# Performance work log

Hardware: AMD Instinct MI355X
Metric: run time of the kernel (lower is better)

## Reference

```python
import jax, jax.numpy as jnp
import numpy as np

EPS = 1e-5
NUM_GROUPS = 32
NUM_HEADS = 8

def group_norm(x, w, b):
    # x: (B, C, H, W), 32 groups, affine per-channel
    B, C, H, W = x.shape
    xg = x.reshape(B, NUM_GROUPS, C // NUM_GROUPS, H, W)
    mu = xg.mean(axis=(2, 3, 4), keepdims=True)
    var = xg.var(axis=(2, 3, 4), keepdims=True)
    xn = ((xg - mu) * jax.lax.rsqrt(var + EPS)).reshape(B, C, H, W)
    return xn * w[None, :, None, None] + b[None, :, None, None]

def conv1x1(x, w, b):
    # 1x1 conv == per-pixel linear; w: (out, in), x: (B, C, H, W)
    return jnp.einsum('oc,bchw->bohw', w, x) + b[None, :, None, None]

def setup_inputs() -> dict:
    key = jax.random.key(0)
    ks = jax.random.split(key, 4)
    B, C, H, W = 2, 512, 64, 64
    s = 1.0 / np.sqrt(C)
    return {
        'x': jax.random.normal(ks[0], (B, C, H, W), jnp.float32),
        'gn_w': jnp.ones((C,), jnp.float32),
        'gn_b': jnp.zeros((C,), jnp.float32),
        'wq': jax.random.normal(ks[1], (C, C), jnp.float32) * s,
        'bq': jnp.zeros((C,), jnp.float32),
        'wkv': jax.random.normal(ks[2], (2 * C, C), jnp.float32) * s,
        'bkv': jnp.zeros((2 * C,), jnp.float32),
        'wo': jax.random.normal(ks[3], (C, C), jnp.float32) * s,
        'bo': jnp.zeros((C,), jnp.float32),
    }

def reference(x, gn_w, gn_b, wq, bq, wkv, bkv, wo, bo):
    B, C, H, W = x.shape
    hd = C // NUM_HEADS  # head_dim
    residual = x
    x_norm = group_norm(x, gn_w, gn_b)
    q = conv1x1(x_norm, wq, bq).reshape(B, NUM_HEADS, hd, H * W)
    kv = conv1x1(x_norm, wkv, bkv)
    k, v = jnp.split(kv, 2, axis=1)
    k = k.reshape(B, NUM_HEADS, hd, H * W)
    v = v.reshape(B, NUM_HEADS, hd, H * W)
    scale = hd ** (-0.5)
    attn = jnp.einsum('bhdi,bhdj->bhij', q, k) * scale
    attn = jax.nn.softmax(attn, axis=-1)
    out = jnp.einsum('bhij,bhdj->bhdi', attn, v).reshape(B, C, H, W)
    out = conv1x1(out, wo, bo)
    return out + residual
```

## Files before the change

kernel.cpp:

```cpp
#include <hip/hip_runtime.h>
#include <cmath>

typedef __bf16 bf16x8 __attribute__((ext_vector_type(8)));
typedef __bf16 bf16x4 __attribute__((ext_vector_type(4)));
typedef float  f32x4  __attribute__((ext_vector_type(4)));
typedef unsigned uint2_ev __attribute__((ext_vector_type(2)));

static __device__ __forceinline__ f32x4 mfma16(bf16x8 a, bf16x8 b, f32x4 c) {
    return __builtin_amdgcn_mfma_f32_16x16x32_bf16(a, b, c, 0, 0, 0);
}

static __device__ __forceinline__ float fast_exp2(float x) {
#if __has_builtin(__builtin_amdgcn_exp2f)
    return __builtin_amdgcn_exp2f(x);
#else
    return exp2f(x);
#endif
}

static __device__ __forceinline__ void quad_swap(unsigned &a, unsigned &b) {
#if __has_builtin(__builtin_amdgcn_permlane32_swap) && __has_builtin(__builtin_amdgcn_permlane16_swap)
    uint2_ev r32 = __builtin_amdgcn_permlane32_swap(a, b, false, false);
    uint2_ev r16 = __builtin_amdgcn_permlane16_swap(r32[0], r32[1], false, false);
    a = r16[0]; b = r16[1];
#else
    asm volatile("v_permlane32_swap_b32 %0, %1\n\t"
                 "v_permlane16_swap_b32 %0, %1"
                 : "+v"(a), "+v"(b));
#endif
}

static __device__ __forceinline__ void gload_lds16(const void* g, void* l) {
    __builtin_amdgcn_global_load_lds((const __attribute__((address_space(1))) void*)g,
                                     (__attribute__((address_space(3))) void*)l, 16, 0, 0);
}

#define OFF_STATS 0
#define OFF_W     4096
#define OFF_XNT   (OFF_W + 2u*1024*1024)
#define OFF_QKT   (OFF_XNT + 8u*1024*1024)
#define OFF_V     (OFF_QKT + 16u*1024*1024)
#define OFF_OP    (OFF_V + 8u*1024*1024)
#define CHUNK_O   4194304u
#define CHUNK_L   65536u

__global__ __launch_bounds__(256) void cvt_w(const float* __restrict__ wq,
                                             const float* __restrict__ wkv,
                                             const float* __restrict__ wo,
                                             __bf16* __restrict__ dst) {
    int i = blockIdx.x * 256 + threadIdx.x;
    if (i < 262144)      dst[i] = (__bf16)wq[i];
    else if (i < 786432) dst[i] = (__bf16)wkv[i - 262144];
    else                 dst[i] = (__bf16)wo[i - 786432];
}

__global__ __launch_bounds__(256) void gn_stats(const float* __restrict__ x,
                                                float* __restrict__ stats) {
    int blk = blockIdx.x;
    int bg = blk >> 2, chunk = blk & 3;
    const float* base = x + (size_t)bg * 65536 + (size_t)chunk * 16384;
    float s = 0.f, ss = 0.f;
    for (int i = threadIdx.x; i < 4096; i += 256) {
        float4 v = ((const float4*)base)[i];
        s  += v.x + v.y + v.z + v.w;
        ss += v.x*v.x + v.y*v.y + v.z*v.z + v.w*v.w;
    }
    #pragma unroll
    for (int off = 1; off < 64; off <<= 1) {
        s  += __shfl_xor(s,  off);
        ss += __shfl_xor(ss, off);
    }
    __shared__ float red[8];
    int wave = threadIdx.x >> 6;
    if ((threadIdx.x & 63) == 0) { red[wave*2] = s; red[wave*2+1] = ss; }
    __syncthreads();
    if (threadIdx.x == 0) {
        float S  = red[0] + red[2] + red[4] + red[6];
        float SS = red[1] + red[3] + red[5] + red[7];
        atomicAdd(&stats[bg*2],     S);
        atomicAdd(&stats[bg*2 + 1], SS);
    }
}

__global__ __launch_bounds__(256) void gn_apply(const float* __restrict__ x,
                                                const float* __restrict__ stats,
                                                const float* __restrict__ w,
                                                const float* __restrict__ bgn,
                                                __bf16* __restrict__ xnT) {
    int p0 = blockIdx.x * 64, c0 = blockIdx.y * 64, b = blockIdx.z;
    int tid = threadIdx.x, lane = tid & 63, wave = tid >> 6;
    __shared__ float t[64][69];
    #pragma unroll
    for (int i = 0; i < 16; ++i) {
        int cc = i * 4 + wave;
        int c  = c0 + cc;
        int g  = (b << 5) + (c >> 4);
        float mu  = stats[g*2] * (1.f/65536.f);
        float var = stats[g*2+1] * (1.f/65536.f) - mu*mu;
        float rstd = rsqrtf(var + 1e-5f);
        float val = x[((size_t)(b*512 + c) << 12) + p0 + lane];
        t[cc][lane] = (val - mu) * rstd * w[c] + bgn[c];
    }
    __syncthreads();
    #pragma unroll
    for (int i = 0; i < 16; ++i) {
        int pp = i * 4 + wave;
        xnT[((size_t)(b*4096 + p0 + pp) << 9) + c0 + lane] = (__bf16)t[lane][pp];
    }
}

__global__ __launch_bounds__(256) void gemm128_kernel(
    const __bf16* __restrict__ A, const __bf16* __restrict__ B,
    const float* __restrict__ bias, const float* __restrict__ bias2, int nsplit,
    float scale0, void* __restrict__ out,
    int N, int K, long long strideA, long long strideO) {
    const int bz = blockIdx.z;
    A += strideA * bz;
    const int m0 = blockIdx.x * 128, n0 = blockIdx.y * 128;
    const int tid = threadIdx.x, lane = tid & 63, wave = tid >> 6;
    const int quad = lane >> 4, l16 = lane & 15;
    const int wm = (wave >> 1) * 64, wn = (wave & 1) * 64;

    __shared__ __attribute__((aligned(16))) __bf16 lds_a[128][40];
    __shared__ __attribute__((aligned(16))) __bf16 lds_b[128][40];

    f32x4 acc[4][4];
    #pragma unroll
    for (int mt = 0; mt < 4; ++mt)
        #pragma unroll
        for (int nt = 0; nt < 4; ++nt)
            #pragma unroll
            for (int r = 0; r < 4; ++r) acc[mt][nt][r] = 0.f;

    const int row_s = tid >> 2;
    const int kc    = (tid & 3) << 3;

    uint4 ra0, ra1, rb0, rb1;
    const __bf16* Abase = A + (size_t)(m0 + row_s) * K + kc;
    const __bf16* Bbase = B + (size_t)(n0 + row_s) * K + kc;
    ra0 = *(const uint4*)Abase;
    ra1 = *(const uint4*)(Abase + (size_t)64 * K);
    rb0 = *(const uint4*)Bbase;
    rb1 = *(const uint4*)(Bbase + (size_t)64 * K);

    for (int kt = 0; kt < K; kt += 32) {
        *(uint4*)&lds_a[row_s][kc]      = ra0;
        *(uint4*)&lds_a[row_s + 64][kc] = ra1;
        *(uint4*)&lds_b[row_s][kc]      = rb0;
        *(uint4*)&lds_b[row_s + 64][kc] = rb1;
        __syncthreads();
        if (kt + 32 < K) {
            ra0 = *(const uint4*)(Abase + kt + 32);
            ra1 = *(const uint4*)(Abase + kt + 32 + (size_t)64 * K);
            rb0 = *(const uint4*)(Bbase + kt + 32);
            rb1 = *(const uint4*)(Bbase + kt + 32 + (size_t)64 * K);
        }
        bf16x8 af[4], bfr[4];
        #pragma unroll
        for (int mt = 0; mt < 4; ++mt)
            af[mt] = *(const bf16x8*)&lds_a[wm + mt*16 + l16][quad*8];
        #pragma unroll
        for (int nt = 0; nt < 4; ++nt)
            bfr[nt] = *(const bf16x8*)&lds_b[wn + nt*16 + l16][quad*8];
        #pragma unroll
        for (int mt = 0; mt < 4; ++mt)
            #pragma unroll
            for (int nt = 0; nt < 4; ++nt)
                acc[mt][nt] = mfma16(af[mt], bfr[nt], acc[mt][nt]);
        __syncthreads();
    }

    #pragma unroll
    for (int mt = 0; mt < 4; ++mt) {
        const int mrow = m0 + wm + mt*16 + quad*4;
        #pragma unroll
        for (int nt = 0; nt < 4; ++nt) {
            const int ncol = n0 + wn + nt*16 + l16;
            #pragma unroll
            for (int r = 0; r < 4; ++r) {
                const int m = mrow + r;
                float bval = (ncol < nsplit) ? bias[ncol] : bias2[ncol - nsplit];
                float val = acc[mt][nt][r] + bval;
                if (ncol < nsplit) val *= scale0;
                ((__bf16*)out)[(size_t)strideO * bz + (size_t)m * N + ncol] = (__bf16)val;
            }
        }
    }
}

template<int OUT_F32, int HAS_RES>
__global__ __launch_bounds__(256) void gemm64_kernel(
    const __bf16* __restrict__ A, const __bf16* __restrict__ B,
    const float* __restrict__ bias, const float* __restrict__ res,
    void* __restrict__ out,
    int N, int K, long long strideB, long long strideO) {
    const int bz = blockIdx.z;
    B += strideB * bz;
    const int m0 = blockIdx.x * 64, n0 = blockIdx.y * 128;
    const int tid = threadIdx.x, lane = tid & 63, wave = tid >> 6;
    const int quad = lane >> 4, l16 = lane & 15;
    const int wn = wave * 32;

    __shared__ __attribute__((aligned(16))) __bf16 lds_a[64][40];
    __shared__ __attribute__((aligned(16))) __bf16 lds_b[128][40];

    f32x4 acc[4][2];
    #pragma unroll
    for (int mt = 0; mt < 4; ++mt)
        #pragma unroll
        for (int nt = 0; nt < 2; ++nt)
            #pragma unroll
            for (int r = 0; r < 4; ++r) acc[mt][nt][r] = 0.f;

    const int row_s = tid >> 2;
    const int kc    = (tid & 3) << 3;

    uint4 ra0, rb0, rb1;
    const __bf16* Abase = A + (size_t)(m0 + row_s) * K + kc;
    const __bf16* Bbase = B + (size_t)(n0 + row_s) * K + kc;
    ra0 = *(const uint4*)Abase;
    rb0 = *(const uint4*)Bbase;
    rb1 = *(const uint4*)(Bbase + (size_t)64 * K);

    for (int kt = 0; kt < K; kt += 32) {
        *(uint4*)&lds_a[row_s][kc]      = ra0;
        *(uint4*)&lds_b[row_s][kc]      = rb0;
        *(uint4*)&lds_b[row_s + 64][kc] = rb1;
        __syncthreads();
        if (kt + 32 < K) {
            ra0 = *(const uint4*)(Abase + kt + 32);
            rb0 = *(const uint4*)(Bbase + kt + 32);
            rb1 = *(const uint4*)(Bbase + kt + 32 + (size_t)64 * K);
        }
        bf16x8 af[4], bfr[2];
        #pragma unroll
        for (int mt = 0; mt < 4; ++mt)
            af[mt] = *(const bf16x8*)&lds_a[mt*16 + l16][quad*8];
        #pragma unroll
        for (int nt = 0; nt < 2; ++nt)
            bfr[nt] = *(const bf16x8*)&lds_b[wn + nt*16 + l16][quad*8];
        #pragma unroll
        for (int mt = 0; mt < 4; ++mt)
            #pragma unroll
            for (int nt = 0; nt < 2; ++nt)
                acc[mt][nt] = mfma16(af[mt], bfr[nt], acc[mt][nt]);
        __syncthreads();
    }

    #pragma unroll
    for (int mt = 0; mt < 4; ++mt) {
        const int mrow = m0 + mt*16 + quad*4;
        #pragma unroll
        for (int nt = 0; nt < 2; ++nt) {
            const int ncol = n0 + wn + nt*16 + l16;
            #pragma unroll
            for (int r = 0; r < 4; ++r) {
                const int m = mrow + r;
                float val = acc[mt][nt][r] + bias[m];
                const size_t idx = (size_t)strideO * bz + (size_t)m * N + ncol;
                if constexpr (HAS_RES) val += res[idx];
                if constexpr (OUT_F32) ((float*)out)[idx] = val;
                else ((__bf16*)out)[idx] = (__bf16)val;
            }
        }
    }
}

template<int NCH>
__global__ __launch_bounds__(256, 3) void attn_kernel(const __bf16* __restrict__ qkT,
                                                      const __bf16* __restrict__ v,
                                                      __bf16* __restrict__ attnT,
                                                      __bf16* __restrict__ Opart,
                                                      float* __restrict__ Lpart) {
    const int b = blockIdx.y >> 3, h = blockIdx.y & 7;
    const int chunk = (NCH > 1) ? blockIdx.z : 0;
    int NITER, kt0;
    if constexpr (NCH == 3) {
        NITER = (chunk == 0) ? 22 : 21;
        kt0   = (chunk == 0) ? 0 : (chunk == 1 ? 1408 : 2752);
    } else {
        NITER = 64 / NCH;
        kt0   = chunk * (4096 / NCH);
    }
    const int tid = threadIdx.x;
    const int wave = tid >> 6, lane = tid & 63;
    const int quad = lane >> 4, l16 = lane & 15;
    const int qbase = blockIdx.x * 256 + wave * 64;

    const __bf16* qkTb = qkT + ((size_t)b << 22);
    const __bf16* vb   = v   + ((size_t)b << 21);

    __shared__ __attribute__((aligned(16))) __bf16 lds_k[2][64][64];
    __shared__ __attribute__((aligned(16))) __bf16 lds_v[2][64][64];

    bf16x8 aq[4][2];
    #pragma unroll
    for (int mt = 0; mt < 4; ++mt) {
        const __bf16* qrow = qkTb + (size_t)(qbase + mt*16 + l16) * 1024 + h*64 + quad*8;
        aq[mt][0] = *(const bf16x8*)qrow;
        aq[mt][1] = *(const bf16x8*)(qrow + 32);
    }
    f32x4 o[4][5];
    #pragma unroll
    for (int mt = 0; mt < 4; ++mt)
        #pragma unroll
        for (int dt = 0; dt < 5; ++dt)
            #pragma unroll
            for (int r = 0; r < 4; ++r) o[mt][dt][r] = 0.f;
    const f32x4 kZero = {0.f, 0.f, 0.f, 0.f};

    bf16x8 onesb;
    #pragma unroll
    for (int e = 0; e < 8; ++e) onesb[e] = (__bf16)1.0f;

    const int myrow = (wave << 3) + (lane >> 3);
    const int mych  = ((lane & 7) ^ (myrow & 7)) << 3;
    const __bf16* kgb = qkTb + (size_t)myrow * 1024 + 512 + h*64 + mych;
    const __bf16* vgb = vb + ((size_t)(h*64 + myrow) << 12) + mych;

    auto stage = [&](int buf, int kt) {
        char* kb = (char*)(&lds_k[buf][0][0]) + (wave << 10);
        char* vp = (char*)(&lds_v[buf][0][0]) + (wave << 10);
        const __bf16* kg = kgb + (size_t)kt * 1024;
        const __bf16* vg = vgb + kt;
        gload_lds16(kg,                       kb);
        gload_lds16(kg + 32*1024,             kb + 4096);
        gload_lds16(vg,                       vp);
        gload_lds16(vg + ((size_t)32 << 12),  vp + 4096);
    };

    stage(0, kt0);

    for (int it = 0; it < NITER; ++it) {
        __syncthreads();
        const int cur = it & 1;
        if (it + 1 < NITER) stage(cur ^ 1, kt0 + (it + 1) * 64);

        #pragma unroll
        for (int kh = 0; kh < 2; ++kh) {
            unsigned pd[4][4];
            #pragma unroll
            for (int j = 0; j < 2; ++j) {
                const int nt = kh*2 + j;
                const int kr = nt*16 + l16;
                bf16x8 bk0 = *(const bf16x8*)&lds_k[cur][kr][( quad      ^ (l16 & 7)) * 8];
                bf16x8 bk1 = *(const bf16x8*)&lds_k[cur][kr][((4 + quad) ^ (l16 & 7)) * 8];
                #pragma unroll
                for (int mt = 0; mt < 4; ++mt) {
                    f32x4 s = mfma16(bk1, aq[mt][1], mfma16(bk0, aq[mt][0], kZero));
                    f32x4 p;
                    #pragma unroll
                    for (int r = 0; r < 4; ++r) p[r] = fast_exp2(s[r]);
                    bf16x4 pb = __builtin_convertvector(p, bf16x4);
                    union { bf16x4 v; unsigned d[2]; } u; u.v = pb;
                    pd[mt][j*2]     = u.d[0];
                    pd[mt][j*2 + 1] = u.d[1];
                }
            }
            bf16x8 pa[4];
            #pragma unroll
            for (int mt = 0; mt < 4; ++mt) {
                unsigned x0 = pd[mt][0], x1 = pd[mt][1];
                unsigned y0 = pd[mt][2], y1 = pd[mt][3];
                quad_swap(x0, y0);
                quad_swap(x1, y1);
                union { unsigned d[4]; bf16x8 v; } u;
                u.d[0] = x0; u.d[1] = x1; u.d[2] = y0; u.d[3] = y1;
                pa[mt] = u.v;
            }
            #pragma unroll
            for (int dt = 0; dt < 4; ++dt) {
                bf16x8 bv = *(const bf16x8*)&lds_v[cur][dt*16 + l16][((kh*4 + quad) ^ (l16 & 7)) * 8];
                #pragma unroll
                for (int mt = 0; mt < 4; ++mt)
                    o[mt][dt] = mfma16(pa[mt], bv, o[mt][dt]);
            }
            #pragma unroll
            for (int mt = 0; mt < 4; ++mt)
                o[mt][4] = mfma16(pa[mt], onesb, o[mt][4]);
        }
    }

    if constexpr (NCH > 1) {
        __bf16* Ob = Opart + (size_t)chunk * CHUNK_O;
        #pragma unroll
        for (int mt = 0; mt < 4; ++mt)
            #pragma unroll
            for (int dt = 0; dt < 4; ++dt)
                #pragma unroll
                for (int r = 0; r < 4; ++r) {
                    size_t row = (size_t)b * 4096 + qbase + mt*16 + quad*4 + r;
                    Ob[(row << 9) + (h << 6) + dt*16 + l16] = (__bf16)o[mt][dt][r];
                }
        if (l16 == 0) {
            #pragma unroll
            for (int mt = 0; mt < 4; ++mt)
                #pragma unroll
                for (int r = 0; r < 4; ++r) {
                    int p = qbase + mt*16 + quad*4 + r;
                    Lpart[(size_t)chunk * CHUNK_L + (size_t)(((b*8 + h)) << 12) + p] = o[mt][4][r];
                }
        }
    } else {
        #pragma unroll
        for (int mt = 0; mt < 4; ++mt) {
            float inv[4];
            #pragma unroll
            for (int r = 0; r < 4; ++r)
                inv[r] = 1.f / __shfl(o[mt][4][r], lane & 48);
            #pragma unroll
            for (int dt = 0; dt < 4; ++dt)
                #pragma unroll
                for (int r = 0; r < 4; ++r) {
                    size_t row = (size_t)b * 4096 + qbase + mt*16 + quad*4 + r;
                    attnT[(row << 9) + (h << 6) + dt*16 + l16] = (__bf16)(o[mt][dt][r] * inv[r]);
                }
        }
    }
}

template<int NCH>
__global__ __launch_bounds__(256) void attn_combine(const __bf16* __restrict__ Opart,
                                                    const float* __restrict__ Lpart,
                                                    __bf16* __restrict__ attnT) {
    int i = blockIdx.x * 256 + threadIdx.x;
    int c4 = i & 127;
    int p  = (i >> 7) & 4095;
    int b  = i >> 19;
    int h  = c4 >> 4;
    size_t lidx = (size_t)((b*8 + h) << 12) + p;
    float l = 0.f;
    #pragma unroll
    for (int ch = 0; ch < NCH; ++ch) l += Lpart[(size_t)ch * CHUNK_L + lidx];
    float inv = 1.f / l;
    size_t oi = ((size_t)(b*4096 + p) << 9) + c4*4;
    float acc[4] = {0.f, 0.f, 0.f, 0.f};
    #pragma unroll
    for (int ch = 0; ch < NCH; ++ch) {
        bf16x4 ov = *(const bf16x4*)&Opart[(size_t)ch * CHUNK_O + oi];
        #pragma unroll
        for (int r = 0; r < 4; ++r) acc[r] += (float)ov[r];
    }
    bf16x4 rv;
    #pragma unroll
    for (int r = 0; r < 4; ++r) rv[r] = (__bf16)(acc[r] * inv);
    *(bf16x4*)&attnT[oi] = rv;
}

extern "C" void kernel_launch(void* const* d_in, const int* in_sizes, int n_in,
                              void* d_out, int out_size, void* d_ws, size_t ws_size,
                              hipStream_t stream) {
    const float* x   = (const float*)d_in[0];
    const float* gnw = (const float*)d_in[1];
    const float* gnb = (const float*)d_in[2];
    const float* wq  = (const float*)d_in[3];
    const float* bq  = (const float*)d_in[4];
    const float* wkv = (const float*)d_in[5];
    const float* bkv = (const float*)d_in[6];
    const float* wo  = (const float*)d_in[7];
    const float* bo  = (const float*)d_in[8];
    float* out = (float*)d_out;

    char* ws = (char*)d_ws;
    float*  stats  = (float*)(ws + OFF_STATS);
    __bf16* wbf    = (__bf16*)(ws + OFF_W);
    __bf16* wkv_bf = wbf + 262144;
    __bf16* wo_bf  = wbf + 786432;
    __bf16* xnT    = (__bf16*)(ws + OFF_XNT);
    __bf16* qkT    = (__bf16*)(ws + OFF_QKT);
    __bf16* vv     = (__bf16*)(ws + OFF_V);
    __bf16* Opart  = (__bf16*)(ws + OFF_OP);
    __bf16* attnT  = xnT;

    const size_t need3 = (size_t)OFF_OP + 3u * (CHUNK_O * 2 + CHUNK_L * 4);
    const size_t need2 = (size_t)OFF_OP + 2u * (CHUNK_O * 2 + CHUNK_L * 4);
    const int nch = (ws_size >= need3) ? 3 : (ws_size >= need2 ? 2 : 1);
    float* Lpart = (float*)(ws + OFF_OP + (size_t)nch * CHUNK_O * 2);

    hipMemsetAsync(stats, 0, 512, stream);
    cvt_w<<<4096, 256, 0, stream>>>(wq, wkv, wo, wbf);
    gn_stats<<<256, 256, 0, stream>>>(x, stats);
    gn_apply<<<dim3(64, 8, 2), 256, 0, stream>>>(x, stats, gnw, gnb, xnT);

    const long long S = 2097152LL;
    const long long S2 = 4194304LL;
    gemm128_kernel<<<dim3(32, 8, 2), 256, 0, stream>>>(
        xnT, wbf, bq, bkv, 512, 0.125f * 1.44269504f, qkT, 1024, 512, S, S2);
    gemm64_kernel<0,0><<<dim3(8, 32, 2), 256, 0, stream>>>(
        wkv_bf + 262144, xnT, bkv + 512, nullptr, vv, 4096, 512, S, S);

    if (nch == 3) {
        attn_kernel<3><<<dim3(16, 16, 3), 256, 0, stream>>>(qkT, vv, nullptr, Opart, Lpart);
        attn_combine<3><<<4096, 256, 0, stream>>>(Opart, Lpart, attnT);
    } else if (nch == 2) {
        attn_kernel<2><<<dim3(16, 16, 2), 256, 0, stream>>>(qkT, vv, nullptr, Opart, Lpart);
        attn_combine<2><<<4096, 256, 0, stream>>>(Opart, Lpart, attnT);
    } else {
        attn_kernel<1><<<dim3(16, 16, 1), 256, 0, stream>>>(qkT, vv, attnT, nullptr, nullptr);
    }

    gemm64_kernel<1,1><<<dim3(8, 32, 2), 256, 0, stream>>>(
        wo_bf, attnT, bo, x, out, 4096, 512, S, S);
}
```

Baseline: 219.9 us.

## Fold GroupNorm affine into QKV weights and fuse stats with transpose

GroupNorm normalization is folded into per-batch scaled Q/K/V weights and an effective bias, computed in a new prep_w kernel. The GN stats pass and the transpose to bf16 now happen in one kernel, so x is read once instead of twice and two launches are removed. The cost is per-batch weight copies (doubling the QKV weight traffic in the GEMMs) and raw x being quantized to bf16 before normalization, which may affect accuracy if x has large per-group offsets.

New measurement: 218.5 us. Within noise of the previous version (-0.6%).

```diff
diff --git a/kernel.cpp b/kernel.cpp
--- a/kernel.cpp
+++ b/kernel.cpp
@@ -36,86 +36,124 @@
 }
 
 #define OFF_STATS 0
-#define OFF_W     4096
-#define OFF_XNT   (OFF_W + 2u*1024*1024)
+#define OFF_BEFF  1024
+#define OFF_W     16384
+#define OFF_XNT   (4u*1024*1024)
 #define OFF_QKT   (OFF_XNT + 8u*1024*1024)
 #define OFF_V     (OFF_QKT + 16u*1024*1024)
 #define OFF_OP    (OFF_V + 8u*1024*1024)
 #define CHUNK_O   4194304u
 #define CHUNK_L   65536u
 
-__global__ __launch_bounds__(256) void cvt_w(const float* __restrict__ wq,
-                                             const float* __restrict__ wkv,
-                                             const float* __restrict__ wo,
-                                             __bf16* __restrict__ dst) {
-    int i = blockIdx.x * 256 + threadIdx.x;
-    if (i < 262144)      dst[i] = (__bf16)wq[i];
-    else if (i < 786432) dst[i] = (__bf16)wkv[i - 262144];
-    else                 dst[i] = (__bf16)wo[i - 786432];
-}
-
-__global__ __launch_bounds__(256) void gn_stats(const float* __restrict__ x,
-                                                float* __restrict__ stats) {
-    int blk = blockIdx.x;
-    int bg = blk >> 2, chunk = blk & 3;
-    const float* base = x + (size_t)bg * 65536 + (size_t)chunk * 16384;
-    float s = 0.f, ss = 0.f;
-    for (int i = threadIdx.x; i < 4096; i += 256) {
-        float4 v = ((const float4*)base)[i];
-        s  += v.x + v.y + v.z + v.w;
-        ss += v.x*v.x + v.y*v.y + v.z*v.z + v.w*v.w;
-    }
-    #pragma unroll
-    for (int off = 1; off < 64; off <<= 1) {
-        s  += __shfl_xor(s,  off);
-        ss += __shfl_xor(ss, off);
-    }
-    __shared__ float red[8];
-    int wave = threadIdx.x >> 6;
-    if ((threadIdx.x & 63) == 0) { red[wave*2] = s; red[wave*2+1] = ss; }
-    __syncthreads();
-    if (threadIdx.x == 0) {
-        float S  = red[0] + red[2] + red[4] + red[6];
-        float SS = red[1] + red[3] + red[5] + red[7];
-        atomicAdd(&stats[bg*2],     S);
-        atomicAdd(&stats[bg*2 + 1], SS);
-    }
-}
-
-__global__ __launch_bounds__(256) void gn_apply(const float* __restrict__ x,
-                                                const float* __restrict__ stats,
-                                                const float* __restrict__ w,
-                                                const float* __restrict__ bgn,
-                                                __bf16* __restrict__ xnT) {
+__global__ __launch_bounds__(256) void gn_fuse(const float* __restrict__ x,
+                                               float* __restrict__ stats,
+                                               __bf16* __restrict__ xT) {
     int p0 = blockIdx.x * 64, c0 = blockIdx.y * 64, b = blockIdx.z;
     int tid = threadIdx.x, lane = tid & 63, wave = tid >> 6;
     __shared__ float t[64][69];
+    __shared__ float red[4][8];
+    float acc_s[4] = {0.f,0.f,0.f,0.f}, acc_ss[4] = {0.f,0.f,0.f,0.f};
     #pragma unroll
     for (int i = 0; i < 16; ++i) {
-        int cc = i * 4 + wave;
-        int c  = c0 + cc;
-        int g  = (b << 5) + (c >> 4);
-        float mu  = stats[g*2] * (1.f/65536.f);
-        float var = stats[g*2+1] * (1.f/65536.f) - mu*mu;
+        int cc = i*4 + wave;
+        float val = x[((size_t)(b*512 + c0 + cc) << 12) + p0 + lane];
+        t[cc][lane] = val;
+        acc_s[i>>2]  += val;
+        acc_ss[i>>2] += val*val;
+    }
+    #pragma unroll
+    for (int g = 0; g < 4; ++g) {
+        #pragma unroll
+        for (int off = 1; off < 64; off <<= 1) {
+            acc_s[g]  += __shfl_xor(acc_s[g],  off);
+            acc_ss[g] += __shfl_xor(acc_ss[g], off);
+        }
+    }
+    if (lane == 0) {
+        #pragma unroll
+        for (int g = 0; g < 4; ++g) { red[wave][g*2] = acc_s[g]; red[wave][g*2+1] = acc_ss[g]; }
+    }
+    __syncthreads();
+    if (tid < 8) {
+        float v0 = red[0][tid] + red[1][tid] + red[2][tid] + red[3][tid];
+        int g = (b << 5) + (c0 >> 4) + (tid >> 1);
+        atomicAdd(&stats[g*2 + (tid & 1)], v0);
+    }
+    #pragma unroll
+    for (int i = 0; i < 16; ++i) {
+        int pp = i*4 + wave;
+        xT[((size_t)(b*4096 + p0 + pp) << 9) + c0 + lane] = (__bf16)t[lane][pp];
+    }
+}
+
+__global__ __launch_bounds__(256) void prep_w(const float* __restrict__ wq,
+                                              const float* __restrict__ wkv,
+                                              const float* __restrict__ wo,
+                                              const float* __restrict__ bq,
+                                              const float* __restrict__ bkv,
+                                              const float* __restrict__ stats,
+                                              const float* __restrict__ gw,
+                                              const float* __restrict__ gb,
+                                              __bf16* __restrict__ wS,
+                                              __bf16* __restrict__ wo_bf,
+                                              float* __restrict__ beff) {
+    const int b = blockIdx.y, bx = blockIdx.x;
+    const int tid = threadIdx.x, lane = tid & 63, wave = tid >> 6;
+    if (bx >= 48) {
+        if (b) return;
+        int r0 = (bx - 48) * 32;
+        #pragma unroll
+        for (int ps = 0; ps < 8; ++ps) {
+            int row = r0 + ps*4 + wave;
+            __bf16 obuf[8];
+            #pragma unroll
+            for (int e = 0; e < 8; ++e) obuf[e] = (__bf16)wo[(size_t)row*512 + lane*8 + e];
+            *(bf16x8*)&wo_bf[(size_t)row*512 + lane*8] = *(bf16x8*)obuf;
+        }
+        return;
+    }
+    __shared__ float sS[512], sT[512];
+    for (int c = tid; c < 512; c += 256) {
+        int g = (b << 5) + (c >> 4);
+        float mu   = stats[g*2] * (1.f/65536.f);
+        float var  = stats[g*2+1] * (1.f/65536.f) - mu*mu;
         float rstd = rsqrtf(var + 1e-5f);
-        float val = x[((size_t)(b*512 + c) << 12) + p0 + lane];
-        t[cc][lane] = (val - mu) * rstd * w[c] + bgn[c];
+        float s = rstd * gw[c];
+        sS[c] = s;
+        sT[c] = gb[c] - mu * s;
     }
     __syncthreads();
-    #pragma unroll
-    for (int i = 0; i < 16; ++i) {
-        int pp = i * 4 + wave;
-        xnT[((size_t)(b*4096 + p0 + pp) << 9) + c0 + lane] = (__bf16)t[lane][pp];
+    int r0 = bx * 32;
+    #pragma unroll
+    for (int ps = 0; ps < 8; ++ps) {
+        int row = r0 + ps*4 + wave;
+        const float* Wrow = (row < 512) ? (wq + (size_t)row*512) : (wkv + (size_t)(row-512)*512);
+        float bias0 = (row < 512) ? bq[row] : bkv[row - 512];
+        float bp = 0.f;
+        __bf16 obuf[8];
+        #pragma unroll
+        for (int e = 0; e < 8; ++e) {
+            int c = lane*8 + e;
+            float wv_ = Wrow[c];
+            obuf[e] = (__bf16)(wv_ * sS[c]);
+            bp += wv_ * sT[c];
+        }
+        *(bf16x8*)&wS[((size_t)b*1536 + row)*512 + lane*8] = *(bf16x8*)obuf;
+        #pragma unroll
+        for (int off = 1; off < 64; off <<= 1) bp += __shfl_xor(bp, off);
+        if (lane == 0) beff[b*1536 + row] = bias0 + bp;
     }
 }
 
 __global__ __launch_bounds__(256) void gemm128_kernel(
     const __bf16* __restrict__ A, const __bf16* __restrict__ B,
-    const float* __restrict__ bias, const float* __restrict__ bias2, int nsplit,
+    const float* __restrict__ bias, int nsplit,
     float scale0, void* __restrict__ out,
-    int N, int K, long long strideA, long long strideO) {
+    int N, int K, long long strideA, long long strideB, long long strideO, int biasStride) {
     const int bz = blockIdx.z;
     A += strideA * bz;
+    B += strideB * bz;
+    const float* bb = bias + (size_t)bz * biasStride;
     const int m0 = blockIdx.x * 128, n0 = blockIdx.y * 128;
     const int tid = threadIdx.x, lane = tid & 63, wave = tid >> 6;
     const int quad = lane >> 4, l16 = lane & 15;
@@ -179,8 +217,7 @@
             #pragma unroll
             for (int r = 0; r < 4; ++r) {
                 const int m = mrow + r;
-                float bval = (ncol < nsplit) ? bias[ncol] : bias2[ncol - nsplit];
-                float val = acc[mt][nt][r] + bval;
+                float val = acc[mt][nt][r] + bb[ncol];
                 if (ncol < nsplit) val *= scale0;
                 ((__bf16*)out)[(size_t)strideO * bz + (size_t)m * N + ncol] = (__bf16)val;
             }
@@ -193,9 +230,11 @@
     const __bf16* __restrict__ A, const __bf16* __restrict__ B,
     const float* __restrict__ bias, const float* __restrict__ res,
     void* __restrict__ out,
-    int N, int K, long long strideB, long long strideO) {
+    int N, int K, long long strideA, long long strideB, long long strideO, int biasStride) {
     const int bz = blockIdx.z;
+    A += strideA * bz;
     B += strideB * bz;
+    const float* bb = bias + (size_t)bz * biasStride;
     const int m0 = blockIdx.x * 64, n0 = blockIdx.y * 128;
     const int tid = threadIdx.x, lane = tid & 63, wave = tid >> 6;
     const int quad = lane >> 4, l16 = lane & 15;
@@ -256,7 +295,7 @@
             #pragma unroll
             for (int r = 0; r < 4; ++r) {
                 const int m = mrow + r;
-                float val = acc[mt][nt][r] + bias[m];
+                float val = acc[mt][nt][r] + bb[m];
                 const size_t idx = (size_t)strideO * bz + (size_t)m * N + ncol;
                 if constexpr (HAS_RES) val += res[idx];
                 if constexpr (OUT_F32) ((float*)out)[idx] = val;
@@ -463,14 +502,14 @@
 
     char* ws = (char*)d_ws;
     float*  stats  = (float*)(ws + OFF_STATS);
-    __bf16* wbf    = (__bf16*)(ws + OFF_W);
-    __bf16* wkv_bf = wbf + 262144;
-    __bf16* wo_bf  = wbf + 786432;
-    __bf16* xnT    = (__bf16*)(ws + OFF_XNT);
+    float*  beff   = (float*)(ws + OFF_BEFF);
+    __bf16* wS     = (__bf16*)(ws + OFF_W);
+    __bf16* wo_bf  = wS + 2u*1536*512;
+    __bf16* xT     = (__bf16*)(ws + OFF_XNT);
     __bf16* qkT    = (__bf16*)(ws + OFF_QKT);
     __bf16* vv     = (__bf16*)(ws + OFF_V);
     __bf16* Opart  = (__bf16*)(ws + OFF_OP);
-    __bf16* attnT  = xnT;
+    __bf16* attnT  = xT;
 
     const size_t need3 = (size_t)OFF_OP + 3u * (CHUNK_O * 2 + CHUNK_L * 4);
     const size_t need2 = (size_t)OFF_OP + 2u * (CHUNK_O * 2 + CHUNK_L * 4);
@@ -478,16 +517,17 @@
     float* Lpart = (float*)(ws + OFF_OP + (size_t)nch * CHUNK_O * 2);
 
     hipMemsetAsync(stats, 0, 512, stream);
-    cvt_w<<<4096, 256, 0, stream>>>(wq, wkv, wo, wbf);
-    gn_stats<<<256, 256, 0, stream>>>(x, stats);
-    gn_apply<<<dim3(64, 8, 2), 256, 0, stream>>>(x, stats, gnw, gnb, xnT);
-
-    const long long S = 2097152LL;
+    gn_fuse<<<dim3(64, 8, 2), 256, 0, stream>>>(x, stats, xT);
+    prep_w<<<dim3(64, 2), 256, 0, stream>>>(wq, wkv, wo, bq, bkv, stats, gnw, gnb,
+                                            wS, wo_bf, beff);
+
+    const long long S  = 2097152LL;
     const long long S2 = 4194304LL;
+    const long long SW = 1536LL*512;
     gemm128_kernel<<<dim3(32, 8, 2), 256, 0, stream>>>(
-        xnT, wbf, bq, bkv, 512, 0.125f * 1.44269504f, qkT, 1024, 512, S, S2);
+        xT, wS, beff, 512, 0.125f * 1.44269504f, qkT, 1024, 512, S, SW, S2, 1536);
     gemm64_kernel<0,0><<<dim3(8, 32, 2), 256, 0, stream>>>(
-        wkv_bf + 262144, xnT, bkv + 512, nullptr, vv, 4096, 512, S, S);
+        wS + 1024*512, xT, beff + 1024, nullptr, vv, 4096, 512, SW, S, S, 1536);
 
     if (nch == 3) {
         attn_kernel<3><<<dim3(16, 16, 3), 256, 0, stream>>>(qkT, vv, nullptr, Opart, Lpart);
@@ -500,5 +540,5 @@
     }
 
     gemm64_kernel<1,1><<<dim3(8, 32, 2), 256, 0, stream>>>(
-        wo_bf, attnT, bo, x, out, 4096, 512, S, S);
-}
+        wo_bf, attnT, bo, x, out, 4096, 512, 0, S, S, 0);
+}
```
